# Kernel tuning notes

Measured on AMD Instinct MI355X. Metric: run time of the kernel, lower is better.

Reference implementation:

```python
import jax, jax.numpy as jnp
import numpy as np


def setup_inputs() -> dict:
    key = jax.random.key(0)
    k1, k2, k3 = jax.random.split(key, 3)
    B, C, H, Wd = 32, 768, 32, 32
    K, DQ = 64, 16
    features = jax.random.normal(k1, (B, C, H, Wd), dtype=jnp.float32)
    query = jax.random.normal(k2, (B, DQ, H, Wd), dtype=jnp.float32)
    # Ensemble of 1x1 convs (bias=False): weight [K, dim_query, dim]
    W = jax.random.normal(k3, (K, DQ, C), dtype=jnp.float32) * (1.0 / np.sqrt(C))
    return {"features": features, "query": query, "W": W}


def reference(features, query, W):
    # Ensemble 1x1 conv: key_values [K, B, DQ, H, W]
    kv = jnp.einsum('bchw,kqc->kbqhw', features, W)
    K, B = kv.shape[0], kv.shape[1]
    # cdist between query (b, 1, d) and keys (b, k, d), d = DQ*H*W
    q_flat = query.reshape(B, -1)                       # [B, D]
    k_flat = jnp.moveaxis(kv.reshape(K, B, -1), 0, 1)   # [B, K, D]
    diff = q_flat[:, None, :] - k_flat                  # [B, K, D]
    distance = jnp.sqrt(jnp.sum(diff * diff, axis=-1))  # [B, K]
    # logits = -distance; codes = argmax(logits) == argmin(distance)
    codes = jnp.argmin(distance, axis=-1)               # [B]
    # per-batch gather of selected key_values
    sel = kv[codes, jnp.arange(B)]                      # [B, DQ, H, W]
    commit_loss = jnp.mean((sel - query) ** 2)
    return sel, codes, commit_loss
```

## Files before the change

kernel.cpp:

```cpp
#include <hip/hip_runtime.h>
#include <cstdint>
#include <cstddef>

typedef float f4 __attribute__((ext_vector_type(4)));
typedef float f32x4 __attribute__((ext_vector_type(4)));
typedef short short8 __attribute__((ext_vector_type(8)));
typedef unsigned short u16x8 __attribute__((ext_vector_type(8)));
typedef unsigned short u16x4 __attribute__((ext_vector_type(4)));
typedef unsigned short ushort_t;

#define B_   32
#define C_   768
#define HW_  1024
#define DQ_  16
#define K_   64
#define M_   1024
#define NHWT 16
#define NCT  12
#define NHALF 72

#define CODE_OFF 524288
#define LOSS_OFF 524320

__device__ __forceinline__ unsigned bf16_rne_bits(float x) {
    unsigned u = __builtin_bit_cast(unsigned, x);
    return (u + 0x7FFFu + ((u >> 16) & 1u)) >> 16;
}
__device__ __forceinline__ float bits_to_f32(unsigned hi16) {
    unsigned u = hi16 << 16;
    return __builtin_bit_cast(float, u);
}
__device__ __forceinline__ void split_bf16(float x, unsigned short& hi, unsigned short& lo) {
    unsigned h = bf16_rne_bits(x);
    hi = (unsigned short)h;
    float r = x - bits_to_f32(h);
    lo = (unsigned short)bf16_rne_bits(r);
}


__global__ __launch_bounds__(256)
void k0_splitF(const float* __restrict__ Fp,
               ushort_t* __restrict__ FhiT, ushort_t* __restrict__ FloT)
{
    __shared__ float tile[64][65];
    const int t = threadIdx.x;
    const int ht = blockIdx.x, ct = blockIdx.y, b = blockIdx.z;

#pragma unroll
    for (int rep = 0; rep < 4; ++rep) {
        int idx = rep * 256 + t;
        int c_l = idx >> 4;
        int hwf = (idx & 15) * 4;
        f4 v = *(const f4*)&Fp[((size_t)b * C_ + ct * 64 + c_l) * HW_ + ht * 64 + hwf];
        tile[c_l][hwf + 0] = v.x;
        tile[c_l][hwf + 1] = v.y;
        tile[c_l][hwf + 2] = v.z;
        tile[c_l][hwf + 3] = v.w;
    }
    __syncthreads();

#pragma unroll
    for (int rep = 0; rep < 2; ++rep) {
        int hw_l = (t >> 3) + rep * 32;
        int cg   = (t & 7) * 8;
        unsigned short hi[8], lo[8];
#pragma unroll
        for (int j = 0; j < 8; ++j)
            split_bf16(tile[cg + j][hw_l], hi[j], lo[j]);
        size_t o = (((size_t)(b * NCT + ct)) * HW_ + ht * 64 + hw_l) * 64 + cg;
        *(u16x8*)&FhiT[o] = *(u16x8*)hi;
        *(u16x8*)&FloT[o] = *(u16x8*)lo;
    }
}

__global__ __launch_bounds__(256)
void k0_splitW(const float* __restrict__ Wp,
               ushort_t* __restrict__ Whi, ushort_t* __restrict__ Wlo)
{
    const unsigned gid = blockIdx.x * 256 + threadIdx.x;
    const unsigned base = gid * 4;
    const unsigned m = base / C_;
    const unsigned c = base - m * C_;
    const unsigned ct = c >> 6, cl = c & 63;
    f4 v = *(const f4*)&Wp[base];
    unsigned short hi[4], lo[4];
    split_bf16(v.x, hi[0], lo[0]);
    split_bf16(v.y, hi[1], lo[1]);
    split_bf16(v.z, hi[2], lo[2]);
    split_bf16(v.w, hi[3], lo[3]);
    size_t o = ((size_t)ct * M_ + m) * 64 + cl;
    *(u16x4*)&Whi[o] = *(u16x4*)hi;
    *(u16x4*)&Wlo[o] = *(u16x4*)lo;
}

__global__ __launch_bounds__(512, 1)
void k1_mfma8(const ushort_t* __restrict__ Whi, const ushort_t* __restrict__ Wlo,
              const ushort_t* __restrict__ FhiT, const ushort_t* __restrict__ FloT,
              const float* __restrict__ Qp, float* __restrict__ partial)
{
    __shared__ ushort_t lds[4][16384];

    const int tid  = threadIdx.x;
    const int w    = tid >> 6;
    const int lane = tid & 63;

    const int bid = blockIdx.x;
    const int idx = (bid & 7) * 64 + (bid >> 3);
    const int mt  = idx & 3;
    const int hwt = (idx >> 2) & 3;
    const int b   = idx >> 4;

    const int wm = w >> 2, wn = w & 3;

    const bool isA   = (w < 4);
    const int  wgrp  = w & 3;
    const int  regoff = isA ? 0 : 8192;

    const int q_l  = lane >> 3;
    const int p_l  = lane & 7;
    const int t_l  = p_l ^ (q_l & 7);
    const int rloc_l = 2 * q_l + (t_l >> 2);
    const int ks_l   = t_l & 3;

    const int c15 = lane & 15, d0 = lane >> 4;
    int offA[8], offB[4];
#pragma unroll
    for (int i = 0; i < 8; ++i) {
        int r = wm * 128 + i * 16 + c15;
        int q = r >> 1;
        offA[i] = q * 64 + (((((r & 1) << 2) | d0) ^ (q & 7)) << 3);
    }
#pragma unroll
    for (int j = 0; j < 4; ++j) {
        int r = wn * 64 + j * 16 + c15;
        int q = r >> 1;
        offB[j] = 8192 + q * 64 + (((((r & 1) << 2) | d0) ^ (q & 7)) << 3);
    }

    f32x4 acc[8][4] = {};

#define STAGE_SETUP(GG)                                                                  \
    const int stile = (GG) >> 1, shalf = (GG) & 1;                                       \
    const int sterm = (stile >= 24) ? 2 : ((stile >= 12) ? 1 : 0);                       \
    const int sct   = stile - sterm * 12;                                                \
    const ushort_t* sb;                                                                  \
    if (isA) sb = ((sterm == 1) ? Wlo : Whi) + ((size_t)sct * M_ + mt * 256) * 64;       \
    else     sb = ((sterm == 2) ? FloT : FhiT) + ((size_t)(b * NCT + sct) * HW_ + hwt * 256) * 64; \
    sb += shalf * 32 + (size_t)(wgrp * 64 + rloc_l) * 64 + ks_l * 8;                     \
    ushort_t* Dst = &lds[(GG) & 3][regoff + wgrp * 2048];

#define STAGE1(II)                                                                       \
    __builtin_amdgcn_global_load_lds(                                                    \
        (const __attribute__((address_space(1))) void*)(sb + (II) * 1024),               \
        (__attribute__((address_space(3))) void*)(Dst + (II) * 512),                     \
        16, 0, 0);

#pragma unroll
    for (int h = 0; h < 3; ++h) {
        STAGE_SETUP(h)
        STAGE1(0) STAGE1(1) STAGE1(2) STAGE1(3)
    }
    asm volatile("s_waitcnt vmcnt(8)" ::: "memory");
    __builtin_amdgcn_s_barrier();

    short8 af[4], bf[4];

    for (int g = 0; g < NHALF; ++g) {
        const ushort_t* L = &lds[g & 3][0];
        const int ggw = g + 3;
        const int gg  = (ggw >= NHALF) ? ggw - NHALF : ggw;
        STAGE_SETUP(gg)

#pragma unroll
        for (int i = 0; i < 4; ++i) af[i] = *(const short8*)&L[offA[i]];
#pragma unroll
        for (int j = 0; j < 4; ++j) bf[j] = *(const short8*)&L[offB[j]];
        STAGE1(0) STAGE1(1)
        __builtin_amdgcn_s_barrier();
        asm volatile("s_waitcnt lgkmcnt(0)" ::: "memory");
        __builtin_amdgcn_sched_barrier(0);
        __builtin_amdgcn_s_setprio(1);
#pragma unroll
        for (int i = 0; i < 4; ++i)
#pragma unroll
            for (int j = 0; j < 4; ++j)
                acc[i][j] = __builtin_amdgcn_mfma_f32_16x16x32_bf16(af[i], bf[j], acc[i][j], 0, 0, 0);
        __builtin_amdgcn_s_setprio(0);
        __builtin_amdgcn_sched_barrier(0);
        __builtin_amdgcn_s_barrier();

#pragma unroll
        for (int i = 0; i < 4; ++i) af[i] = *(const short8*)&L[offA[4 + i]];
        STAGE1(2) STAGE1(3)
        __builtin_amdgcn_s_barrier();
        asm volatile("s_waitcnt lgkmcnt(0)" ::: "memory");
        __builtin_amdgcn_sched_barrier(0);
        __builtin_amdgcn_s_setprio(1);
#pragma unroll
        for (int i = 0; i < 4; ++i)
#pragma unroll
            for (int j = 0; j < 4; ++j)
                acc[4 + i][j] = __builtin_amdgcn_mfma_f32_16x16x32_bf16(af[i], bf[j], acc[4 + i][j], 0, 0, 0);
        __builtin_amdgcn_s_setprio(0);
        __builtin_amdgcn_sched_barrier(0);
        asm volatile("s_waitcnt vmcnt(8)" ::: "memory");
        __builtin_amdgcn_s_barrier();
    }
#undef STAGE1
#undef STAGE_SETUP

    float qv[4][4];
#pragma unroll
    for (int j = 0; j < 4; ++j) {
        const int hw = hwt * 256 + wn * 64 + j * 16 + c15;
#pragma unroll
        for (int r = 0; r < 4; ++r)
            qv[j][r] = Qp[(size_t)(b * DQ_ + d0 * 4 + r) * HW_ + hw];
    }
#pragma unroll
    for (int i = 0; i < 8; ++i) {
        float s = 0.f;
#pragma unroll
        for (int j = 0; j < 4; ++j)
#pragma unroll
            for (int r = 0; r < 4; ++r) {
                float d = qv[j][r] - acc[i][j][r];
                s = fmaf(d, d, s);
            }
#pragma unroll
        for (int off = 32; off; off >>= 1) s += __shfl_xor(s, off);
        if (lane == 0) {
            const int k = mt * 16 + wm * 8 + i;
            partial[((size_t)b * K_ + k) * NHWT + hwt * 4 + wn] = s;
        }
    }
}

__global__ __launch_bounds__(1024)
void k2_select(const float* __restrict__ partial, float* __restrict__ out,
               int* __restrict__ codes_ws)
{
    const int tid = threadIdx.x;
    const int b = tid >> 5, kk = tid & 31;
    float s0 = 0.f, s1 = 0.f;
#pragma unroll
    for (int h = 0; h < NHWT; ++h) {
        s0 += partial[((size_t)b * K_ + kk) * NHWT + h];
        s1 += partial[((size_t)b * K_ + kk + 32) * NHWT + h];
    }
    float bv = s0; int bk = kk;
    if (s1 < bv) { bv = s1; bk = kk + 32; }
#pragma unroll
    for (int m = 16; m >= 1; m >>= 1) {
        float ov = __shfl_xor(bv, m);
        int   ok = __shfl_xor(bk, m);
        if (ov < bv || (ov == bv && ok < bk)) { bv = ov; bk = ok; }
    }
    __shared__ float mins[32];
    if (kk == 0) {
        out[CODE_OFF + b] = (float)bk;
        codes_ws[b] = bk;
        mins[b] = bv;
    }
    __syncthreads();
    if (tid == 0) {
        float t = 0.f;
#pragma unroll
        for (int i = 0; i < 32; ++i) t += mins[i];
        out[LOSS_OFF] = t * (1.0f / 524288.0f);
    }
}

__global__ __launch_bounds__(256)
void k3_mfma(const ushort_t* __restrict__ Whi, const ushort_t* __restrict__ Wlo,
             const ushort_t* __restrict__ FhiT, const ushort_t* __restrict__ FloT,
             const int* __restrict__ codes_ws, float* __restrict__ out)
{
    __shared__ ushort_t lds3[2][10240];

    const int tid = threadIdx.x;
    const int w = tid >> 6, lane = tid & 63;
    const int b = blockIdx.x >> 4, hwt = blockIdx.x & 15;
    const int code = codes_ws[b];

    const int srow = lane >> 3, sslot = (lane & 7) ^ srow;
    const int c15 = lane & 15, d0 = lane >> 4;

    int offAhi[2], offAlo[2], offBh[2], offBl[2];
#pragma unroll
    for (int kh = 0; kh < 2; ++kh) {
        const int d = kh * 4 + d0;
        const int mA = c15;
        offAhi[kh] = mA * 64 + ((d ^ (mA & 7)) << 3);
        const int mAl = 16 + c15;
        offAlo[kh] = mAl * 64 + ((d ^ (mAl & 7)) << 3);
        const int rB = w * 16 + c15;
        offBh[kh] = 2048 + rB * 64 + ((d ^ (rB & 7)) << 3);
        offBl[kh] = 6144 + rB * 64 + ((d ^ (rB & 7)) << 3);
    }

#define K3_STAGE(CT, BUF)                                                                        \
    {                                                                                            \
        ushort_t* Lb = &lds3[(BUF)][0];                                                          \
        const ushort_t* bhp = FhiT + ((size_t)(b * NCT + (CT)) * HW_ + hwt * 64) * 64;           \
        const ushort_t* blp = FloT + ((size_t)(b * NCT + (CT)) * HW_ + hwt * 64) * 64;           \
        _Pragma("unroll")                                                                        \
        for (int ii = 0; ii < 2; ++ii) {                                                         \
            __builtin_amdgcn_global_load_lds(                                                    \
                (const __attribute__((address_space(1))) void*)(bhp + (w * 16 + ii * 8 + srow) * 64 + sslot * 8), \
                (__attribute__((address_space(3))) void*)(Lb + 2048 + (w * 16 + ii * 8) * 64),   \
                16, 0, 0);                                                                       \
            __builtin_amdgcn_global_load_lds(                                                    \
                (const __attribute__((address_space(1))) void*)(blp + (w * 16 + ii * 8 + srow) * 64 + sslot * 8), \
                (__attribute__((address_space(3))) void*)(Lb + 6144 + (w * 16 + ii * 8) * 64),   \
                16, 0, 0);                                                                       \
        }                                                                                        \
        if (w == 0) {                                                                            \
            const ushort_t* ahp = Whi + ((size_t)(CT) * M_ + code * 16) * 64;                    \
            _Pragma("unroll")                                                                    \
            for (int ii = 0; ii < 2; ++ii)                                                       \
                __builtin_amdgcn_global_load_lds(                                                \
                    (const __attribute__((address_space(1))) void*)(ahp + (ii * 8 + srow) * 64 + sslot * 8), \
                    (__attribute__((address_space(3))) void*)(Lb + (ii * 8) * 64),               \
                    16, 0, 0);                                                                   \
        } else if (w == 1) {                                                                     \
            const ushort_t* alp = Wlo + ((size_t)(CT) * M_ + code * 16) * 64;                    \
            _Pragma("unroll")                                                                    \
            for (int ii = 0; ii < 2; ++ii)                                                       \
                __builtin_amdgcn_global_load_lds(                                                \
                    (const __attribute__((address_space(1))) void*)(alp + (ii * 8 + srow) * 64 + sslot * 8), \
                    (__attribute__((address_space(3))) void*)(Lb + (16 + ii * 8) * 64),          \
                    16, 0, 0);                                                                   \
        }                                                                                        \
    }

    f32x4 acc = {};

    K3_STAGE(0, 0)
    asm volatile("s_waitcnt vmcnt(0)" ::: "memory");
    __syncthreads();

    for (int ct = 0; ct < NCT; ++ct) {
        const int cur = ct & 1;
        if (ct + 1 < NCT) K3_STAGE(ct + 1, cur ^ 1)
        const ushort_t* L = &lds3[cur][0];
        short8 ah[2], al2[2], bh[2], bl[2];
#pragma unroll
        for (int kh = 0; kh < 2; ++kh) {
            ah[kh]  = *(const short8*)&L[offAhi[kh]];
            al2[kh] = *(const short8*)&L[offAlo[kh]];
            bh[kh]  = *(const short8*)&L[offBh[kh]];
            bl[kh]  = *(const short8*)&L[offBl[kh]];
        }
#pragma unroll
        for (int kh = 0; kh < 2; ++kh) {
            acc = __builtin_amdgcn_mfma_f32_16x16x32_bf16(ah[kh], bh[kh], acc, 0, 0, 0);
            acc = __builtin_amdgcn_mfma_f32_16x16x32_bf16(ah[kh], bl[kh], acc, 0, 0, 0);
            acc = __builtin_amdgcn_mfma_f32_16x16x32_bf16(al2[kh], bh[kh], acc, 0, 0, 0);
        }
        asm volatile("s_waitcnt vmcnt(0)" ::: "memory");
        __syncthreads();
    }
#undef K3_STAGE

#pragma unroll
    for (int r = 0; r < 4; ++r) {
        const int q = d0 * 4 + r;
        out[((size_t)(b * DQ_ + q)) * HW_ + hwt * 64 + w * 16 + c15] = acc[r];
    }
}

#define BM   256
#define BN   64
#define BC   32
#define NMT  4

__global__ __launch_bounds__(256)
void k1_dist_fp32(const float* __restrict__ Fp, const float* __restrict__ Qp,
                  const float* __restrict__ Wp, float* __restrict__ partial)
{
    __shared__ float w_lds[BC][BM];
    __shared__ float f_lds[BC][BN + 8];
    __shared__ float red[32][8];

    const int tid = threadIdx.x;
    const int mt = blockIdx.x, hwt = blockIdx.y, b = blockIdx.z;
    const int ty = tid >> 3, tx = tid & 7;
    const int m0 = ty * 8, hw0 = tx * 8;

    float acc[8][8];
#pragma unroll
    for (int i = 0; i < 8; ++i)
#pragma unroll
        for (int j = 0; j < 8; ++j) acc[i][j] = 0.f;

    for (int c0 = 0; c0 < C_; c0 += BC) {
#pragma unroll
        for (int i = 0; i < 8; ++i) {
            const int m_l = i * 32 + ty;
            const int c_l = tx * 4;
            const int col = m_l ^ (tx * 4);
            f4 w4 = *(const f4*)&Wp[(size_t)(mt * BM + m_l) * C_ + c0 + c_l];
            w_lds[c_l + 0][col] = w4.x;
            w_lds[c_l + 1][col] = w4.y;
            w_lds[c_l + 2][col] = w4.z;
            w_lds[c_l + 3][col] = w4.w;
        }
        {
            const int c = tid >> 3;
            const int hw = (tid & 7) * 8;
            const float* src = &Fp[((size_t)b * C_ + c0 + c) * HW_ + (size_t)hwt * BN + hw];
            *(f4*)&f_lds[c][hw]     = *(const f4*)src;
            *(f4*)&f_lds[c][hw + 4] = *(const f4*)(src + 4);
        }
        __syncthreads();

#pragma unroll 4
        for (int cc = 0; cc < BC; ++cc) {
            const int sw = ((cc >> 2) & 7) * 4;
            const int colA = m0 ^ sw;
            f4 w0 = *(const f4*)&w_lds[cc][colA];
            f4 w1 = *(const f4*)&w_lds[cc][colA ^ 4];
            f4 g0 = *(const f4*)&f_lds[cc][hw0];
            f4 g1 = *(const f4*)&f_lds[cc][hw0 + 4];
            const float wa[8] = {w0.x, w0.y, w0.z, w0.w, w1.x, w1.y, w1.z, w1.w};
            const float fv[8] = {g0.x, g0.y, g0.z, g0.w, g1.x, g1.y, g1.z, g1.w};
#pragma unroll
            for (int i = 0; i < 8; ++i)
#pragma unroll
                for (int j = 0; j < 8; ++j)
                    acc[i][j] = fmaf(wa[i], fv[j], acc[i][j]);
        }
        __syncthreads();
    }

    const int q0 = (ty & 1) * 8;
    float s = 0.f;
#pragma unroll
    for (int i = 0; i < 8; ++i) {
        const float* qp = &Qp[((size_t)b * DQ_ + q0 + i) * HW_ + (size_t)hwt * BN + hw0];
        f4 qa = *(const f4*)qp;
        f4 qb = *(const f4*)(qp + 4);
        float d;
        d = qa.x - acc[i][0]; s = fmaf(d, d, s);
        d = qa.y - acc[i][1]; s = fmaf(d, d, s);
        d = qa.z - acc[i][2]; s = fmaf(d, d, s);
        d = qa.w - acc[i][3]; s = fmaf(d, d, s);
        d = qb.x - acc[i][4]; s = fmaf(d, d, s);
        d = qb.y - acc[i][5]; s = fmaf(d, d, s);
        d = qb.z - acc[i][6]; s = fmaf(d, d, s);
        d = qb.w - acc[i][7]; s = fmaf(d, d, s);
    }
    red[ty][tx] = s;
    __syncthreads();
    if (tid < 16) {
        float t = 0.f;
#pragma unroll
        for (int r = 0; r < 2; ++r)
#pragma unroll
            for (int x = 0; x < 8; ++x) t += red[tid * 2 + r][x];
        partial[((size_t)b * K_ + mt * 16 + tid) * NHWT + hwt] = t;
    }
}

#define BN3 128
#define BC3 32

__global__ __launch_bounds__(256)
void k3_sel(const float* __restrict__ Fp, const float* __restrict__ Wp,
            const int* __restrict__ codes_ws, float* __restrict__ out)
{
    __shared__ float f_lds[BC3][BN3];
    __shared__ float w_lds[DQ_][33];

    const int tid = threadIdx.x;
    const int b = blockIdx.x >> 3, hwt = blockIdx.x & 7;
    const int code = codes_ws[b];
    const int q = tid >> 4;
    const int hw0 = (tid & 15) * 8;

    float a[8] = {0.f, 0.f, 0.f, 0.f, 0.f, 0.f, 0.f, 0.f};

    for (int c0 = 0; c0 < C_; c0 += BC3) {
        if (tid < 128) {
            const int qq = tid >> 3, c4 = (tid & 7) * 4;
            f4 w4 = *(const f4*)&Wp[((size_t)code * DQ_ + qq) * C_ + c0 + c4];
            w_lds[qq][c4 + 0] = w4.x;
            w_lds[qq][c4 + 1] = w4.y;
            w_lds[qq][c4 + 2] = w4.z;
            w_lds[qq][c4 + 3] = w4.w;
        }
        {
            const int c = tid >> 3;
            const int hw = (tid & 7) * 16;
            const float* src = &Fp[((size_t)b * C_ + c0 + c) * HW_ + (size_t)hwt * BN3 + hw];
            *(f4*)&f_lds[c][hw]      = *(const f4*)(src);
            *(f4*)&f_lds[c][hw + 4]  = *(const f4*)(src + 4);
            *(f4*)&f_lds[c][hw + 8]  = *(const f4*)(src + 8);
            *(f4*)&f_lds[c][hw + 12] = *(const f4*)(src + 12);
        }
        __syncthreads();
#pragma unroll 4
        for (int cc = 0; cc < BC3; ++cc) {
            const float wv = w_lds[q][cc];
            f4 g0 = *(const f4*)&f_lds[cc][hw0];
            f4 g1 = *(const f4*)&f_lds[cc][hw0 + 4];
            a[0] = fmaf(wv, g0.x, a[0]);
            a[1] = fmaf(wv, g0.y, a[1]);
            a[2] = fmaf(wv, g0.z, a[2]);
            a[3] = fmaf(wv, g0.w, a[3]);
            a[4] = fmaf(wv, g1.x, a[4]);
            a[5] = fmaf(wv, g1.y, a[5]);
            a[6] = fmaf(wv, g1.z, a[6]);
            a[7] = fmaf(wv, g1.w, a[7]);
        }
        __syncthreads();
    }

    float* dst = &out[((size_t)b * DQ_ + q) * HW_ + (size_t)hwt * BN3 + hw0];
    f4 o0 = {a[0], a[1], a[2], a[3]};
    f4 o1 = {a[4], a[5], a[6], a[7]};
    *(f4*)dst = o0;
    *(f4*)(dst + 4) = o1;
}

extern "C" void kernel_launch(void* const* d_in, const int* in_sizes, int n_in,
                              void* d_out, int out_size, void* d_ws, size_t ws_size,
                              hipStream_t stream)
{
    const float* Fp = (const float*)d_in[0];
    const float* Qp = (const float*)d_in[1];
    const float* Wp = (const float*)d_in[2];
    float* out = (float*)d_out;

    const size_t FT_ELEMS = (size_t)B_ * HW_ * C_;
    const size_t W_ELEMS  = (size_t)M_ * C_;
    const size_t PART_OFF = 4 * FT_ELEMS + 4 * W_ELEMS;
    const size_t CODE_WS  = PART_OFF + (size_t)B_ * K_ * NHWT * 4;
    const size_t NEED     = CODE_WS + 128;

    if (ws_size >= NEED) {
        ushort_t* FhiT = (ushort_t*)d_ws;
        ushort_t* FloT = FhiT + FT_ELEMS;
        ushort_t* Whi  = FloT + FT_ELEMS;
        ushort_t* Wlo  = Whi + W_ELEMS;
        float* partial = (float*)((char*)d_ws + PART_OFF);
        int* codes_ws  = (int*)((char*)d_ws + CODE_WS);

        k0_splitF<<<dim3(16, NCT, B_), 256, 0, stream>>>(Fp, FhiT, FloT);
        k0_splitW<<<dim3(W_ELEMS / 1024), 256, 0, stream>>>(Wp, Whi, Wlo);
        k1_mfma8<<<dim3(512), 512, 0, stream>>>(Whi, Wlo, FhiT, FloT, Qp, partial);
        k2_select<<<1, 1024, 0, stream>>>(partial, out, codes_ws);
        k3_mfma<<<dim3(B_ * 16), 256, 0, stream>>>(Whi, Wlo, FhiT, FloT, codes_ws, out);
    } else {
        float* partial = (float*)d_ws;
        int* codes_ws  = (int*)((char*)d_ws + (size_t)B_ * K_ * NHWT * 4);
        k1_dist_fp32<<<dim3(NMT, NHWT, B_), 256, 0, stream>>>(Fp, Qp, Wp, partial);
        k2_select<<<1, 1024, 0, stream>>>(partial, out, codes_ws);
        k3_sel<<<dim3(B_ * 8), 256, 0, stream>>>(Fp, Wp, codes_ws, out);
    }
}
```

Measured before the change: 322.0 us.

## Switch distance GEMM to 32x32x16 MFMA with 3-stage LDS ring and 2 blocks/CU

Rewrites the main distance kernel to use 32x32x16 bf16 MFMA instead of 16x16x32, with a new LDS layout and swizzle that has 32-element rows. The LDS ring shrinks from 4 to 3 stages, which frees enough shared memory for two 512-thread blocks per CU (launch_bounds 512,2). The main loop is restructured into an unroll-by-3 tile macro, and the epilogue is remapped to the 32x32 accumulator layout, producing two k rows per accumulator. The goal is better MFMA throughput per LDS read and higher occupancy, at the cost of register pressure and a shallower prefetch pipeline.

```diff
diff --git a/kernel.cpp b/kernel.cpp
--- a/kernel.cpp
+++ b/kernel.cpp
@@ -4,6 +4,7 @@
 
 typedef float f4 __attribute__((ext_vector_type(4)));
 typedef float f32x4 __attribute__((ext_vector_type(4)));
+typedef float f32x16 __attribute__((ext_vector_type(16)));
 typedef short short8 __attribute__((ext_vector_type(8)));
 typedef unsigned short u16x8 __attribute__((ext_vector_type(8)));
 typedef unsigned short u16x4 __attribute__((ext_vector_type(4)));
@@ -17,7 +18,7 @@
 #define M_   1024
 #define NHWT 16
 #define NCT  12
-#define NHALF 72
+#define NTILES 72
 
 #define CODE_OFF 524288
 #define LOSS_OFF 524320
@@ -93,12 +94,17 @@
     *(u16x4*)&Wlo[o] = *(u16x4*)lo;
 }
 
-__global__ __launch_bounds__(512, 1)
-void k1_mfma8(const ushort_t* __restrict__ Whi, const ushort_t* __restrict__ Wlo,
-              const ushort_t* __restrict__ FhiT, const ushort_t* __restrict__ FloT,
-              const float* __restrict__ Qp, float* __restrict__ partial)
-{
-    __shared__ ushort_t lds[4][16384];
+#define GLL(SRC, DST)                                                    \
+    __builtin_amdgcn_global_load_lds(                                    \
+        (const __attribute__((address_space(1))) void*)(SRC),            \
+        (__attribute__((address_space(3))) void*)(DST), 16, 0, 0)
+
+__global__ __launch_bounds__(512, 2)
+void k1_mfma32(const ushort_t* __restrict__ Whi, const ushort_t* __restrict__ Wlo,
+               const ushort_t* __restrict__ FhiT, const ushort_t* __restrict__ FloT,
+               const float* __restrict__ Qp, float* __restrict__ partial)
+{
+    __shared__ ushort_t lds[3][16384];
 
     const int tid  = threadIdx.x;
     const int w    = tid >> 6;
@@ -112,126 +118,147 @@
 
     const int wm = w >> 2, wn = w & 3;
 
-    const bool isA   = (w < 4);
-    const int  wgrp  = w & 3;
+    const bool isA    = (w < 4);
+    const int  wgrp   = w & 3;
     const int  regoff = isA ? 0 : 8192;
 
-    const int q_l  = lane >> 3;
-    const int p_l  = lane & 7;
-    const int t_l  = p_l ^ (q_l & 7);
-    const int rloc_l = 2 * q_l + (t_l >> 2);
-    const int ks_l   = t_l & 3;
-
-    const int c15 = lane & 15, d0 = lane >> 4;
-    int offA[8], offB[4];
-#pragma unroll
-    for (int i = 0; i < 8; ++i) {
-        int r = wm * 128 + i * 16 + c15;
-        int q = r >> 1;
-        offA[i] = q * 64 + (((((r & 1) << 2) | d0) ^ (q & 7)) << 3);
-    }
-#pragma unroll
-    for (int j = 0; j < 4; ++j) {
-        int r = wn * 64 + j * 16 + c15;
-        int q = r >> 1;
-        offB[j] = 8192 + q * 64 + (((((r & 1) << 2) | d0) ^ (q & 7)) << 3);
-    }
-
-    f32x4 acc[8][4] = {};
-
-#define STAGE_SETUP(GG)                                                                  \
-    const int stile = (GG) >> 1, shalf = (GG) & 1;                                       \
-    const int sterm = (stile >= 24) ? 2 : ((stile >= 12) ? 1 : 0);                       \
-    const int sct   = stile - sterm * 12;                                                \
-    const ushort_t* sb;                                                                  \
-    if (isA) sb = ((sterm == 1) ? Wlo : Whi) + ((size_t)sct * M_ + mt * 256) * 64;       \
-    else     sb = ((sterm == 2) ? FloT : FhiT) + ((size_t)(b * NCT + sct) * HW_ + hwt * 256) * 64; \
-    sb += shalf * 32 + (size_t)(wgrp * 64 + rloc_l) * 64 + ks_l * 8;                     \
-    ushort_t* Dst = &lds[(GG) & 3][regoff + wgrp * 2048];
-
-#define STAGE1(II)                                                                       \
-    __builtin_amdgcn_global_load_lds(                                                    \
-        (const __attribute__((address_space(1))) void*)(sb + (II) * 1024),               \
-        (__attribute__((address_space(3))) void*)(Dst + (II) * 512),                     \
-        16, 0, 0);
-
-#pragma unroll
-    for (int h = 0; h < 3; ++h) {
-        STAGE_SETUP(h)
-        STAGE1(0) STAGE1(1) STAGE1(2) STAGE1(3)
-    }
-    asm volatile("s_waitcnt vmcnt(8)" ::: "memory");
+    const int srow  = lane >> 2;
+    const int sslot = (lane & 3) ^ (srow & 3);
+
+    const int l31 = lane & 31, hi5 = lane >> 5;
+    int offA[4][2], offB[2][2];
+#pragma unroll
+    for (int i = 0; i < 4; ++i) {
+        const int r = wm * 128 + i * 32 + l31;
+#pragma unroll
+        for (int kh = 0; kh < 2; ++kh) {
+            const int d = kh * 2 + hi5;
+            offA[i][kh] = r * 32 + ((d ^ (r & 3)) << 3);
+        }
+    }
+#pragma unroll
+    for (int j = 0; j < 2; ++j) {
+        const int r = wn * 64 + j * 32 + l31;
+#pragma unroll
+        for (int kh = 0; kh < 2; ++kh) {
+            const int d = kh * 2 + hi5;
+            offB[j][kh] = 8192 + r * 32 + ((d ^ (r & 3)) << 3);
+        }
+    }
+
+    f32x16 acc[4][2] = {};
+
+    {
+        const ushort_t* sb0 = isA ? (Whi + ((size_t)mt * 256) * 64)
+                                  : (FhiT + ((size_t)(b * NCT) * HW_ + hwt * 256) * 64);
+        sb0 += (size_t)(wgrp * 64 + srow) * 64 + sslot * 8;
+#pragma unroll
+        for (int ii = 0; ii < 4; ++ii)
+            GLL(sb0 + ii * 1024, &lds[0][regoff + (wgrp * 64 + ii * 16) * 32]);
+        const ushort_t* sb1 = sb0 + 32;
+#pragma unroll
+        for (int ii = 0; ii < 4; ++ii)
+            GLL(sb1 + ii * 1024, &lds[1][regoff + (wgrp * 64 + ii * 16) * 32]);
+    }
+    asm volatile("s_waitcnt vmcnt(4)" ::: "memory");
     __builtin_amdgcn_s_barrier();
 
-    short8 af[4], bf[4];
-
-    for (int g = 0; g < NHALF; ++g) {
-        const ushort_t* L = &lds[g & 3][0];
-        const int ggw = g + 3;
-        const int gg  = (ggw >= NHALF) ? ggw - NHALF : ggw;
-        STAGE_SETUP(gg)
-
-#pragma unroll
-        for (int i = 0; i < 4; ++i) af[i] = *(const short8*)&L[offA[i]];
-#pragma unroll
-        for (int j = 0; j < 4; ++j) bf[j] = *(const short8*)&L[offB[j]];
-        STAGE1(0) STAGE1(1)
-        __builtin_amdgcn_s_barrier();
-        asm volatile("s_waitcnt lgkmcnt(0)" ::: "memory");
-        __builtin_amdgcn_sched_barrier(0);
-        __builtin_amdgcn_s_setprio(1);
-#pragma unroll
-        for (int i = 0; i < 4; ++i)
-#pragma unroll
-            for (int j = 0; j < 4; ++j)
-                acc[i][j] = __builtin_amdgcn_mfma_f32_16x16x32_bf16(af[i], bf[j], acc[i][j], 0, 0, 0);
-        __builtin_amdgcn_s_setprio(0);
-        __builtin_amdgcn_sched_barrier(0);
-        __builtin_amdgcn_s_barrier();
-
-#pragma unroll
-        for (int i = 0; i < 4; ++i) af[i] = *(const short8*)&L[offA[4 + i]];
-        STAGE1(2) STAGE1(3)
-        __builtin_amdgcn_s_barrier();
-        asm volatile("s_waitcnt lgkmcnt(0)" ::: "memory");
-        __builtin_amdgcn_sched_barrier(0);
-        __builtin_amdgcn_s_setprio(1);
-#pragma unroll
-        for (int i = 0; i < 4; ++i)
-#pragma unroll
-            for (int j = 0; j < 4; ++j)
-                acc[4 + i][j] = __builtin_amdgcn_mfma_f32_16x16x32_bf16(af[i], bf[j], acc[4 + i][j], 0, 0, 0);
-        __builtin_amdgcn_s_setprio(0);
-        __builtin_amdgcn_sched_barrier(0);
-        asm volatile("s_waitcnt vmcnt(8)" ::: "memory");
-        __builtin_amdgcn_s_barrier();
-    }
-#undef STAGE1
-#undef STAGE_SETUP
-
-    float qv[4][4];
-#pragma unroll
-    for (int j = 0; j < 4; ++j) {
-        const int hw = hwt * 256 + wn * 64 + j * 16 + c15;
-#pragma unroll
-        for (int r = 0; r < 4; ++r)
-            qv[j][r] = Qp[(size_t)(b * DQ_ + d0 * 4 + r) * HW_ + hw];
-    }
-#pragma unroll
-    for (int i = 0; i < 8; ++i) {
-        float s = 0.f;
-#pragma unroll
-        for (int j = 0; j < 4; ++j)
-#pragma unroll
-            for (int r = 0; r < 4; ++r) {
-                float d = qv[j][r] - acc[i][j][r];
-                s = fmaf(d, d, s);
+#define TILE(U, U2)                                                                      \
+    {                                                                                    \
+        const int t = it * 3 + (U);                                                      \
+        int tn = t + 2; if (tn >= NTILES) tn -= NTILES;                                  \
+        const int stile = tn >> 1, shalf = tn & 1;                                       \
+        const int term = (stile >= 24) ? 2 : ((stile >= 12) ? 1 : 0);                    \
+        const int sct = stile - term * 12;                                               \
+        const ushort_t* sb;                                                              \
+        if (isA) sb = ((term == 1) ? Wlo : Whi) + ((size_t)sct * M_ + mt * 256) * 64;    \
+        else sb = ((term == 2) ? FloT : FhiT) + ((size_t)(b * NCT + sct) * HW_ + hwt * 256) * 64; \
+        sb += shalf * 32 + (size_t)(wgrp * 64 + srow) * 64 + sslot * 8;                  \
+        const ushort_t* L = &lds[(U)][0];                                                \
+        ushort_t* D = &lds[(U2)][0] + regoff;                                            \
+        short8 av[4], bv[2];                                                             \
+                         \
+        _Pragma("unroll")                                                                \
+        for (int i2 = 0; i2 < 4; ++i2) av[i2] = *(const short8*)&L[offA[i2][0]];         \
+        _Pragma("unroll")                                                                \
+        for (int j2 = 0; j2 < 2; ++j2) bv[j2] = *(const short8*)&L[offB[j2][0]];         \
+        GLL(sb, D + (wgrp * 64 + 0) * 32);                                               \
+        GLL(sb + 1024, D + (wgrp * 64 + 16) * 32);                                       \
+        __builtin_amdgcn_s_barrier();                                                    \
+        asm volatile("s_waitcnt lgkmcnt(0)" ::: "memory");                               \
+        __builtin_amdgcn_sched_barrier(0);                                               \
+        __builtin_amdgcn_s_setprio(1);                                                   \
+        _Pragma("unroll")                                                                \
+        for (int i2 = 0; i2 < 4; ++i2)                                                   \
+            _Pragma("unroll")                                                            \
+            for (int j2 = 0; j2 < 2; ++j2)                                               \
+                acc[i2][j2] = __builtin_amdgcn_mfma_f32_32x32x16_bf16(                   \
+                    av[i2], bv[j2], acc[i2][j2], 0, 0, 0);                               \
+        __builtin_amdgcn_s_setprio(0);                                                   \
+        __builtin_amdgcn_sched_barrier(0);                                               \
+        __builtin_amdgcn_s_barrier();                                                    \
+               \
+        _Pragma("unroll")                                                                \
+        for (int i2 = 0; i2 < 4; ++i2) av[i2] = *(const short8*)&L[offA[i2][1]];         \
+        _Pragma("unroll")                                                                \
+        for (int j2 = 0; j2 < 2; ++j2) bv[j2] = *(const short8*)&L[offB[j2][1]];         \
+        GLL(sb + 2048, D + (wgrp * 64 + 32) * 32);                                       \
+        GLL(sb + 3072, D + (wgrp * 64 + 48) * 32);                                       \
+        __builtin_amdgcn_s_barrier();                                                    \
+        asm volatile("s_waitcnt lgkmcnt(0)" ::: "memory");                               \
+        __builtin_amdgcn_sched_barrier(0);                                               \
+        __builtin_amdgcn_s_setprio(1);                                                   \
+        _Pragma("unroll")                                                                \
+        for (int i2 = 0; i2 < 4; ++i2)                                                   \
+            _Pragma("unroll")                                                            \
+            for (int j2 = 0; j2 < 2; ++j2)                                               \
+                acc[i2][j2] = __builtin_amdgcn_mfma_f32_32x32x16_bf16(                   \
+                    av[i2], bv[j2], acc[i2][j2], 0, 0, 0);                               \
+        __builtin_amdgcn_s_setprio(0);                                                   \
+        __builtin_amdgcn_sched_barrier(0);                                               \
+        asm volatile("s_waitcnt vmcnt(4)" ::: "memory");   \
+        __builtin_amdgcn_s_barrier();                                                    \
+    }
+
+#pragma unroll 1
+    for (int it = 0; it < 24; ++it) {
+        TILE(0, 2)
+        TILE(1, 0)
+        TILE(2, 1)
+    }
+#undef TILE
+
+    float qv[2][8];
+#pragma unroll
+    for (int j = 0; j < 2; ++j) {
+        const int hw = hwt * 256 + wn * 64 + j * 32 + l31;
+#pragma unroll
+        for (int qi = 0; qi < 8; ++qi) {
+            const int q = (qi & 3) + 8 * (qi >> 2) + 4 * hi5;
+            qv[j][qi] = Qp[(size_t)(b * DQ_ + q) * HW_ + hw];
+        }
+    }
+#pragma unroll
+    for (int i = 0; i < 4; ++i) {
+        float s0 = 0.f, s1 = 0.f;
+#pragma unroll
+        for (int j = 0; j < 2; ++j)
+#pragma unroll
+            for (int r = 0; r < 16; ++r) {
+                const int qi = (r & 3) + 4 * ((r >> 2) & 1);
+                const float d = qv[j][qi] - acc[i][j][r];
+                if (r < 8) s0 = fmaf(d, d, s0);
+                else       s1 = fmaf(d, d, s1);
             }
 #pragma unroll
-        for (int off = 32; off; off >>= 1) s += __shfl_xor(s, off);
+        for (int off = 32; off; off >>= 1) {
+            s0 += __shfl_xor(s0, off);
+            s1 += __shfl_xor(s1, off);
+        }
         if (lane == 0) {
-            const int k = mt * 16 + wm * 8 + i;
-            partial[((size_t)b * K_ + k) * NHWT + hwt * 4 + wn] = s;
+            const int k = mt * 16 + wm * 8 + i * 2;
+            partial[((size_t)b * K_ + k) * NHWT + hwt * 4 + wn]     = s0;
+            partial[((size_t)b * K_ + k + 1) * NHWT + hwt * 4 + wn] = s1;
         }
     }
 }
@@ -306,31 +333,21 @@
         const ushort_t* blp = FloT + ((size_t)(b * NCT + (CT)) * HW_ + hwt * 64) * 64;           \
         _Pragma("unroll")                                                                        \
         for (int ii = 0; ii < 2; ++ii) {                                                         \
-            __builtin_amdgcn_global_load_lds(                                                    \
-                (const __attribute__((address_space(1))) void*)(bhp + (w * 16 + ii * 8 + srow) * 64 + sslot * 8), \
-                (__attribute__((address_space(3))) void*)(Lb + 2048 + (w * 16 + ii * 8) * 64),   \
-                16, 0, 0);                                                                       \
-            __builtin_amdgcn_global_load_lds(                                                    \
-                (const __attribute__((address_space(1))) void*)(blp + (w * 16 + ii * 8 + srow) * 64 + sslot * 8), \
-                (__attribute__((address_space(3))) void*)(Lb + 6144 + (w * 16 + ii * 8) * 64),   \
-                16, 0, 0);                                                                       \
+            GLL(bhp + (w * 16 + ii * 8 + srow) * 64 + sslot * 8,                                 \
+                Lb + 2048 + (w * 16 + ii * 8) * 64);                                             \
+            GLL(blp + (w * 16 + ii * 8 + srow) * 64 + sslot * 8,                                 \
+                Lb + 6144 + (w * 16 + ii * 8) * 64);                                             \
         }                                                                                        \
         if (w == 0) {                                                                            \
             const ushort_t* ahp = Whi + ((size_t)(CT) * M_ + code * 16) * 64;                    \
             _Pragma("unroll")                                                                    \
             for (int ii = 0; ii < 2; ++ii)                                                       \
-                __builtin_amdgcn_global_load_lds(                                                \
-                    (const __attribute__((address_space(1))) void*)(ahp + (ii * 8 + srow) * 64 + sslot * 8), \
-                    (__attribute__((address_space(3))) void*)(Lb + (ii * 8) * 64),               \
-                    16, 0, 0);                                                                   \
+                GLL(ahp + (ii * 8 + srow) * 64 + sslot * 8, Lb + (ii * 8) * 64);                 \
         } else if (w == 1) {                                                                     \
             const ushort_t* alp = Wlo + ((size_t)(CT) * M_ + code * 16) * 64;                    \
             _Pragma("unroll")                                                                    \
             for (int ii = 0; ii < 2; ++ii)                                                       \
-                __builtin_amdgcn_global_load_lds(                                                \
-                    (const __attribute__((address_space(1))) void*)(alp + (ii * 8 + srow) * 64 + sslot * 8), \
-                    (__attribute__((address_space(3))) void*)(Lb + (16 + ii * 8) * 64),          \
-                    16, 0, 0);                                                                   \
+                GLL(alp + (ii * 8 + srow) * 64 + sslot * 8, Lb + (16 + ii * 8) * 64);            \
         }                                                                                        \
     }
 
@@ -549,7 +566,7 @@
 
         k0_splitF<<<dim3(16, NCT, B_), 256, 0, stream>>>(Fp, FhiT, FloT);
         k0_splitW<<<dim3(W_ELEMS / 1024), 256, 0, stream>>>(Wp, Whi, Wlo);
-        k1_mfma8<<<dim3(512), 512, 0, stream>>>(Whi, Wlo, FhiT, FloT, Qp, partial);
+        k1_mfma32<<<dim3(512), 512, 0, stream>>>(Whi, Wlo, FhiT, FloT, Qp, partial);
         k2_select<<<1, 1024, 0, stream>>>(partial, out, codes_ws);
         k3_mfma<<<dim3(B_ * 16), 256, 0, stream>>>(Whi, Wlo, FhiT, FloT, codes_ws, out);
     } else {
```

New measurement: 351.2 us. +9.1%, slower.
